# Kernel optimization log

Measured on AMD Instinct MI355X. Metric: run time of the kernel, lower is better.

## Reference

```python
import jax, jax.numpy as jnp
import numpy as np

N = 20000      # total nodes
E = 320000     # edges before self loops
G = 64         # graphs in the batch
H = 8          # attention heads
NEG_SLOPE = 0.2
EPS = 1e-5


def _gatv2(x, src, dst, Wl, bl, Wr, br, att, bias, concat):
    # PyG GATv2Conv: xl = lin_l(x) (source/messages), xr = lin_r(x) (target)
    heads, C = att.shape
    xl = (x @ Wl + bl).reshape(-1, heads, C)
    xr = (x @ Wr + br).reshape(-1, heads, C)
    e = jax.nn.leaky_relu(xl[src] + xr[dst], NEG_SLOPE)          # [E', H, C]
    a = jnp.einsum('ehc,hc->eh', e, att)                          # [E', H]
    amax = jax.ops.segment_max(a, dst, num_segments=N)
    a = jnp.exp(a - amax[dst])
    a = a / jax.ops.segment_sum(a, dst, num_segments=N)[dst]
    out = jax.ops.segment_sum(xl[src] * a[..., None], dst, num_segments=N)
    out = out.reshape(-1, heads * C) if concat else out.mean(axis=1)
    return out + bias


def _graphnorm(x, batch, w, b, ms):
    cnt = jnp.maximum(jax.ops.segment_sum(jnp.ones((x.shape[0],), x.dtype), batch, num_segments=G), 1.0)[:, None]
    mean = jax.ops.segment_sum(x, batch, num_segments=G) / cnt
    out = x - mean[batch] * ms
    var = jax.ops.segment_sum(out * out, batch, num_segments=G) / cnt
    return w * out / jnp.sqrt(var + EPS)[batch] + b


def _mean_pool(x, batch):
    cnt = jnp.maximum(jax.ops.segment_sum(jnp.ones((x.shape[0],), x.dtype), batch, num_segments=G), 1.0)[:, None]
    return jax.ops.segment_sum(x, batch, num_segments=G) / cnt


def setup_inputs():
    key = jax.random.key(0)
    ks = iter(jax.random.split(key, 40))

    def gl(shape, scale=0.05):
        return jax.random.normal(next(ks), shape, jnp.float32) * scale

    inp = {}
    inp['x'] = jax.random.normal(next(ks), (N, 19), jnp.float32)
    inp['edge_index'] = jax.random.randint(next(ks), (2, E), 0, N, jnp.int32)
    inp['batch'] = jnp.sort(jax.random.randint(next(ks), (N,), 0, G, jnp.int32))

    # layer 1: 19 -> (8 heads x 32), concat -> 256
    inp['W1l'] = gl((19, 256)); inp['b1l'] = jnp.zeros((256,), jnp.float32)
    inp['W1r'] = gl((19, 256)); inp['b1r'] = jnp.zeros((256,), jnp.float32)
    inp['att1'] = gl((H, 32)); inp['bias1'] = jnp.zeros((256,), jnp.float32)
    inp['gn1_w'] = jnp.ones((256,), jnp.float32); inp['gn1_b'] = jnp.zeros((256,), jnp.float32); inp['gn1_ms'] = jnp.ones((256,), jnp.float32)

    inp['W2l'] = gl((256, 128)); inp['b2l'] = jnp.zeros((128,), jnp.float32)
    inp['W2r'] = gl((256, 128)); inp['b2r'] = jnp.zeros((128,), jnp.float32)
    inp['att2'] = gl((H, 16)); inp['bias2'] = jnp.zeros((128,), jnp.float32)
    inp['gn2_w'] = jnp.ones((128,), jnp.float32); inp['gn2_b'] = jnp.zeros((128,), jnp.float32); inp['gn2_ms'] = jnp.ones((128,), jnp.float32)

    inp['W3l'] = gl((128, 64)); inp['b3l'] = jnp.zeros((64,), jnp.float32)
    inp['W3r'] = gl((128, 64)); inp['b3r'] = jnp.zeros((64,), jnp.float32)
    inp['att3'] = gl((H, 8)); inp['bias3'] = jnp.zeros((8,), jnp.float32)
    inp['gn3_w'] = jnp.ones((8,), jnp.float32); inp['gn3_b'] = jnp.zeros((8,), jnp.float32); inp['gn3_ms'] = jnp.ones((8,), jnp.float32)

    inp['lin_w'] = gl((8, 4)); inp['lin_b'] = jnp.zeros((4,), jnp.float32)
    return inp


def reference(x, edge_index, batch, W1l, b1l, W1r, b1r, att1, bias1, gn1_w, gn1_b, gn1_ms,
              W2l, b2l, W2r, b2r, att2, bias2, gn2_w, gn2_b, gn2_ms,
              W3l, b3l, W3r, b3r, att3, bias3, gn3_w, gn3_b, gn3_ms, lin_w, lin_b):
    loop = jnp.arange(N, dtype=edge_index.dtype)  # GATv2Conv add_self_loops=True
    src = jnp.concatenate([edge_index[0], loop])
    dst = jnp.concatenate([edge_index[1], loop])

    h = _gatv2(x, src, dst, W1l, b1l, W1r, b1r, att1, bias1, True)
    h = jax.nn.relu(_graphnorm(h, batch, gn1_w, gn1_b, gn1_ms))
    h = _gatv2(h, src, dst, W2l, b2l, W2r, b2r, att2, bias2, True)
    h = jax.nn.relu(_graphnorm(h, batch, gn2_w, gn2_b, gn2_ms))
    h = _gatv2(h, src, dst, W3l, b3l, W3r, b3r, att3, bias3, False)
    h = jax.nn.relu(_graphnorm(h, batch, gn3_w, gn3_b, gn3_ms))

    features = _mean_pool(h, batch)        # [G, 8]
    logits = features @ lin_w + lin_b      # [G, 4]
    return (logits, features)
```

## Files before the change

kernel.cpp:

```cpp
#include <hip/hip_runtime.h>
#include <math.h>

#define NN 20000
#define EE 320000
#define GG 64
#define HH 8
#define EPSV 1e-5f

static inline unsigned int gridFor(long n, int b){ return (unsigned int)((n + b - 1)/b); }

typedef __attribute__((ext_vector_type(8))) short short8;
typedef __attribute__((ext_vector_type(4))) float f32x4;
typedef unsigned short ushort_t;

__global__ void k_deg(const int* __restrict__ edst, int* __restrict__ deg){
    int e = blockIdx.x*blockDim.x + threadIdx.x;
    if (e < EE) atomicAdd(&deg[edst[e]], 1);
}

__global__ void k_scan(const int* __restrict__ deg, int* __restrict__ indptr){
    __shared__ int partial[1024];
    const int CH = (NN + 1023)/1024;
    int t = threadIdx.x;
    int base = t*CH;
    int vals[CH];
    int sum = 0;
    for (int i = 0; i < CH; ++i){
        int v = (base+i < NN) ? deg[base+i] : 0;
        vals[i] = sum; sum += v;
    }
    partial[t] = sum;
    __syncthreads();
    for (int off = 1; off < 1024; off <<= 1){
        int v = (t >= off) ? partial[t-off] : 0;
        __syncthreads();
        partial[t] += v;
        __syncthreads();
    }
    int prefix = (t > 0) ? partial[t-1] : 0;
    for (int i = 0; i < CH; ++i)
        if (base+i < NN) indptr[base+i] = prefix + vals[i];
    if (t == 1023) indptr[NN] = prefix + sum;
}

__global__ void k_scatter(const int* __restrict__ esrc, const int* __restrict__ edst,
                          const int* __restrict__ indptr, int* __restrict__ cursor,
                          int* __restrict__ srclist){
    int e = blockIdx.x*blockDim.x + threadIdx.x;
    if (e >= EE) return;
    int d = edst[e];
    int pos = atomicAdd(&cursor[d], 1);
    srclist[indptr[d] + pos] = esrc[e];
}

__global__ void k_bounds(const int* __restrict__ batch, int* __restrict__ gstart, int* __restrict__ gend){
    int i = blockIdx.x*blockDim.x + threadIdx.x;
    if (i >= NN) return;
    int b = batch[i];
    if (i == 0 || batch[i-1] != b) gstart[b] = i;
    if (i == NN-1 || batch[i+1] != b) gend[b] = i+1;
}

__device__ __forceinline__ float asf(unsigned int u){
    union{unsigned int i; float f;} c; c.i = u; return c.f;
}
__device__ __forceinline__ ushort_t f2bf(float x){
    unsigned u = __float_as_uint(x);
    unsigned r = u + 0x7FFFu + ((u >> 16) & 1u);
    return (ushort_t)(r >> 16);
}
__device__ __forceinline__ void split_bf16(float x, short& hi, short& lo){
    unsigned u = __float_as_uint(x);
    unsigned r = u + 0x7FFFu + ((u >> 16) & 1u);
    hi = (short)(r >> 16);
    float hf = asf(((unsigned)(unsigned short)hi) << 16);
    float res = x - hf;
    unsigned u2 = __float_as_uint(res);
    unsigned r2 = u2 + 0x7FFFu + ((u2 >> 16) & 1u);
    lo = (short)(r2 >> 16);
}

#define SA 40

template<bool NORM>
__global__ __launch_bounds__(256)
void k_gemm_mfma(const float* __restrict__ h,
                 const float* __restrict__ Wl, const float* __restrict__ bl,
                 const float* __restrict__ Wr, const float* __restrict__ br,
                 const float* __restrict__ gmu, const float* __restrict__ ginv,
                 const float* __restrict__ nw, const float* __restrict__ nb,
                 const int* __restrict__ batch,
                 ushort_t* __restrict__ xlb, float* __restrict__ xr,
                 int K, int HC){
    __shared__ short Ahi[64*SA], Alo[64*SA], Bhi[64*SA], Blo[64*SA];
    const int tid  = threadIdx.x;
    const int lane = tid & 63;
    const int wave = tid >> 6;
    const int m0   = blockIdx.x * 64;
    const int n0g  = blockIdx.y * 64;
    const bool right = (n0g >= HC);
    const float* W  = right ? Wr : Wl;
    const float* bv = right ? br : bl;
    const int nbase = right ? (n0g - HC) : n0g;

    const int wr = (wave & 1) * 32;
    const int wc = (wave >> 1) * 32;

    f32x4 acc[2][2] = {};

    const int sm = tid & 63;
    const int sq = tid >> 6;
    const bool kvec = ((K & 7) == 0);

    for (int k0 = 0; k0 < K; k0 += 32){
        {
            int gm = m0 + sm;
            int kb = k0 + sq*8;
            float v[8];
            if (gm < NN && kvec && kb + 8 <= K){
                const float* src = h + (long)gm*K + kb;
                float4 t0 = *(const float4*)src;
                float4 t1 = *(const float4*)(src+4);
                v[0]=t0.x; v[1]=t0.y; v[2]=t0.z; v[3]=t0.w;
                v[4]=t1.x; v[5]=t1.y; v[6]=t1.z; v[7]=t1.w;
            } else {
                const float* src = h + (long)gm*K + kb;
                #pragma unroll
                for (int j = 0; j < 8; ++j)
                    v[j] = (gm < NN && kb + j < K) ? src[j] : 0.f;
            }
            if (NORM && gm < NN){
                int g = batch[gm];
                const float* mu = gmu + (long)g*K;
                const float* iv = ginv + (long)g*K;
                #pragma unroll
                for (int j = 0; j < 8; ++j){
                    int c = kb + j;
                    float t = (v[j] - mu[c]) * iv[c] * nw[c] + nb[c];
                    v[j] = fmaxf(t, 0.f);
                }
            }
            short hi[8], lo[8];
            #pragma unroll
            for (int j = 0; j < 8; ++j) split_bf16(v[j], hi[j], lo[j]);
            *(short8*)&Ahi[sm*SA + sq*8] = *(short8*)hi;
            *(short8*)&Alo[sm*SA + sq*8] = *(short8*)lo;
        }
        {
            int n = sm;
            float v[8];
            #pragma unroll
            for (int j = 0; j < 8; ++j){
                int gk = k0 + sq*8 + j;
                v[j] = (gk < K) ? W[(long)gk*HC + nbase + n] : 0.f;
            }
            short hi[8], lo[8];
            #pragma unroll
            for (int j = 0; j < 8; ++j) split_bf16(v[j], hi[j], lo[j]);
            *(short8*)&Bhi[n*SA + sq*8] = *(short8*)hi;
            *(short8*)&Blo[n*SA + sq*8] = *(short8*)lo;
        }
        __syncthreads();

        const int fm = lane & 15;
        const int fk = (lane >> 4) * 8;
        short8 ah0 = *(short8*)&Ahi[(wr+fm)*SA + fk];
        short8 ah1 = *(short8*)&Ahi[(wr+16+fm)*SA + fk];
        short8 al0 = *(short8*)&Alo[(wr+fm)*SA + fk];
        short8 al1 = *(short8*)&Alo[(wr+16+fm)*SA + fk];
        short8 bh0 = *(short8*)&Bhi[(wc+fm)*SA + fk];
        short8 bh1 = *(short8*)&Bhi[(wc+16+fm)*SA + fk];
        short8 bl0 = *(short8*)&Blo[(wc+fm)*SA + fk];
        short8 bl1 = *(short8*)&Blo[(wc+16+fm)*SA + fk];

        acc[0][0] = __builtin_amdgcn_mfma_f32_16x16x32_bf16(al0, bh0, acc[0][0], 0,0,0);
        acc[0][0] = __builtin_amdgcn_mfma_f32_16x16x32_bf16(ah0, bl0, acc[0][0], 0,0,0);
        acc[0][0] = __builtin_amdgcn_mfma_f32_16x16x32_bf16(ah0, bh0, acc[0][0], 0,0,0);
        acc[0][1] = __builtin_amdgcn_mfma_f32_16x16x32_bf16(al0, bh1, acc[0][1], 0,0,0);
        acc[0][1] = __builtin_amdgcn_mfma_f32_16x16x32_bf16(ah0, bl1, acc[0][1], 0,0,0);
        acc[0][1] = __builtin_amdgcn_mfma_f32_16x16x32_bf16(ah0, bh1, acc[0][1], 0,0,0);
        acc[1][0] = __builtin_amdgcn_mfma_f32_16x16x32_bf16(al1, bh0, acc[1][0], 0,0,0);
        acc[1][0] = __builtin_amdgcn_mfma_f32_16x16x32_bf16(ah1, bl0, acc[1][0], 0,0,0);
        acc[1][0] = __builtin_amdgcn_mfma_f32_16x16x32_bf16(ah1, bh0, acc[1][0], 0,0,0);
        acc[1][1] = __builtin_amdgcn_mfma_f32_16x16x32_bf16(al1, bh1, acc[1][1], 0,0,0);
        acc[1][1] = __builtin_amdgcn_mfma_f32_16x16x32_bf16(ah1, bl1, acc[1][1], 0,0,0);
        acc[1][1] = __builtin_amdgcn_mfma_f32_16x16x32_bf16(ah1, bh1, acc[1][1], 0,0,0);

        __syncthreads();
    }

    #pragma unroll
    for (int i = 0; i < 2; ++i){
        int row0 = m0 + wr + i*16 + (lane >> 4)*4;
        #pragma unroll
        for (int j = 0; j < 2; ++j){
            int col = wc + j*16 + (lane & 15);
            float bb = bv[nbase + col];
            #pragma unroll
            for (int r = 0; r < 4; ++r){
                int gm = row0 + r;
                if (gm >= NN) continue;
                float v = acc[i][j][r] + bb;
                if (right) xr[(long)gm*HC + nbase + col] = v;
                else       xlb[(long)gm*HC + nbase + col] = f2bf(v);
            }
        }
    }
}

template<int VEC> struct VT;
template<> struct VT<1>{ using T = float;  };
template<> struct VT<2>{ using T = float2; };
template<> struct VT<4>{ using T = float4; };

template<int VEC> struct BF;
template<> struct BF<1>{
    static __device__ __forceinline__ float load(const ushort_t* p){
        return asf(((unsigned)*p) << 16);
    }
};
template<> struct BF<2>{
    static __device__ __forceinline__ float2 load(const ushort_t* p){
        unsigned u = *(const unsigned*)p;
        return make_float2(asf(u << 16), asf(u & 0xFFFF0000u));
    }
};
template<> struct BF<4>{
    static __device__ __forceinline__ float4 load(const ushort_t* p){
        uint2 u = *(const uint2*)p;
        return make_float4(asf(u.x << 16), asf(u.x & 0xFFFF0000u),
                           asf(u.y << 16), asf(u.y & 0xFFFF0000u));
    }
};

__device__ __forceinline__ float lrelu(float z){ return z > 0.f ? z : 0.2f*z; }

__device__ __forceinline__ float edot(float xv, float xr, float at){
    return lrelu(xv + xr) * at;
}
__device__ __forceinline__ float edot(float2 xv, float2 xr, float2 at){
    return lrelu(xv.x+xr.x)*at.x + lrelu(xv.y+xr.y)*at.y;
}
__device__ __forceinline__ float edot(float4 xv, float4 xr, float4 at){
    return lrelu(xv.x+xr.x)*at.x + lrelu(xv.y+xr.y)*at.y
         + lrelu(xv.z+xr.z)*at.z + lrelu(xv.w+xr.w)*at.w;
}
__device__ __forceinline__ void efma(float& o, float p, float xv){ o = fmaf(p,xv,o); }
__device__ __forceinline__ void efma(float2& o, float p, float2 xv){
    o.x = fmaf(p,xv.x,o.x); o.y = fmaf(p,xv.y,o.y);
}
__device__ __forceinline__ void efma(float4& o, float p, float4 xv){
    o.x = fmaf(p,xv.x,o.x); o.y = fmaf(p,xv.y,o.y);
    o.z = fmaf(p,xv.z,o.z); o.w = fmaf(p,xv.w,o.w);
}
__device__ __forceinline__ float escale(float o, float s, float b){ return fmaf(o,s,b); }
__device__ __forceinline__ float2 escale(float2 o, float s, float2 b){
    return make_float2(fmaf(o.x,s,b.x), fmaf(o.y,s,b.y));
}
__device__ __forceinline__ float4 escale(float4 o, float s, float4 b){
    return make_float4(fmaf(o.x,s,b.x), fmaf(o.y,s,b.y), fmaf(o.z,s,b.z), fmaf(o.w,s,b.w));
}

__device__ __forceinline__ float red8(float v){
    v += __shfl_xor(v, 1);
    v += __shfl_xor(v, 2);
    v += __shfl_xor(v, 4);
    return v;
}

template<int VEC, bool MEAN>
__global__ __launch_bounds__(256)
void k_gat_w(const int* __restrict__ indptr, const int* __restrict__ srclist,
             const ushort_t* __restrict__ xlb, const float* __restrict__ xr,
             const float* __restrict__ att, const float* __restrict__ bias,
             float* __restrict__ val){
    using V = typename VT<VEC>::T;
    constexpr int HC = 64*VEC;
    const int lane = threadIdx.x & 63;
    const int d = blockIdx.x*4 + (threadIdx.x >> 6);
    const int co = lane*VEC;

    V xrd = *(const V*)&xr[(long)d*HC + co];
    V at  = *(const V*)&att[co];
    V xls = BF<VEC>::load(xlb + (long)d*HC + co);

    float m0 = red8(edot(xls, xrd, at));
    float l = 1.0f;
    V o = xls;

    int j = indptr[d], end = indptr[d+1];
    for (; j + 8 <= end; j += 8){
        int s0 = srclist[j+0], s1 = srclist[j+1], s2 = srclist[j+2], s3 = srclist[j+3];
        int s4 = srclist[j+4], s5 = srclist[j+5], s6 = srclist[j+6], s7 = srclist[j+7];
        V x0 = BF<VEC>::load(xlb + (long)s0*HC + co);
        V x1 = BF<VEC>::load(xlb + (long)s1*HC + co);
        V x2 = BF<VEC>::load(xlb + (long)s2*HC + co);
        V x3 = BF<VEC>::load(xlb + (long)s3*HC + co);
        V x4 = BF<VEC>::load(xlb + (long)s4*HC + co);
        V x5 = BF<VEC>::load(xlb + (long)s5*HC + co);
        V x6 = BF<VEC>::load(xlb + (long)s6*HC + co);
        V x7 = BF<VEC>::load(xlb + (long)s7*HC + co);
        float a0 = red8(edot(x0, xrd, at));
        float a1 = red8(edot(x1, xrd, at));
        float a2 = red8(edot(x2, xrd, at));
        float a3 = red8(edot(x3, xrd, at));
        float a4 = red8(edot(x4, xrd, at));
        float a5 = red8(edot(x5, xrd, at));
        float a6 = red8(edot(x6, xrd, at));
        float a7 = red8(edot(x7, xrd, at));
        float p0 = __expf(a0 - m0), p1 = __expf(a1 - m0);
        float p2 = __expf(a2 - m0), p3 = __expf(a3 - m0);
        float p4 = __expf(a4 - m0), p5 = __expf(a5 - m0);
        float p6 = __expf(a6 - m0), p7 = __expf(a7 - m0);
        l += ((p0+p1)+(p2+p3)) + ((p4+p5)+(p6+p7));
        efma(o, p0, x0); efma(o, p1, x1); efma(o, p2, x2); efma(o, p3, x3);
        efma(o, p4, x4); efma(o, p5, x5); efma(o, p6, x6); efma(o, p7, x7);
    }
    for (; j < end; j += 4){
        int m = end - j;
        int s0 = srclist[j];
        int s1 = (m > 1) ? srclist[j+1] : s0;
        int s2 = (m > 2) ? srclist[j+2] : s0;
        int s3 = (m > 3) ? srclist[j+3] : s0;
        V x0 = BF<VEC>::load(xlb + (long)s0*HC + co);
        V x1 = BF<VEC>::load(xlb + (long)s1*HC + co);
        V x2 = BF<VEC>::load(xlb + (long)s2*HC + co);
        V x3 = BF<VEC>::load(xlb + (long)s3*HC + co);
        float a0 = red8(edot(x0, xrd, at));
        float a1 = red8(edot(x1, xrd, at));
        float a2 = red8(edot(x2, xrd, at));
        float a3 = red8(edot(x3, xrd, at));
        float p0 = __expf(a0 - m0);
        float p1 = __expf(a1 - m0);
        float p2 = __expf(a2 - m0);
        float p3 = __expf(a3 - m0);
        l += p0; efma(o, p0, x0);
        if (m > 1){ l += p1; efma(o, p1, x1); }
        if (m > 2){ l += p2; efma(o, p2, x2); }
        if (m > 3){ l += p3; efma(o, p3, x3); }
    }
    float invl = 1.0f / l;
    if (!MEAN){
        V bv = *(const V*)&bias[co];
        *(V*)&val[(long)d*HC + co] = escale(o, invl, bv);
    } else {
        float r = ((float&)o) * invl;
        r += __shfl_xor(r, 8);
        r += __shfl_xor(r, 16);
        r += __shfl_xor(r, 32);
        if (lane < 8) val[(long)d*8 + lane] = r*0.125f + bias[lane];
    }
}

template<int F>
__global__ void k_gn_partial(const float* __restrict__ val,
                             const int* __restrict__ gstart, const int* __restrict__ gend,
                             float* __restrict__ gsum, float* __restrict__ gsq){
    int g = blockIdx.x, ch = blockIdx.y, nch = gridDim.y;
    int c = threadIdx.x;
    int s = gstart[g], e = gend[g];
    float sum = 0.f, sq = 0.f;
    for (int i = s + ch; i < e; i += nch){
        float v = val[(long)i*F + c];
        sum += v; sq += v*v;
    }
    if (sum != 0.f || sq != 0.f){
        atomicAdd(&gsum[g*F + c], sum);
        atomicAdd(&gsq[g*F + c], sq);
    }
}

__global__ void k_gn_finalize(const float* __restrict__ gsum, const float* __restrict__ gsq,
                              const int* __restrict__ gstart, const int* __restrict__ gend,
                              const float* __restrict__ ms,
                              float* __restrict__ gmu, float* __restrict__ ginv, int F){
    int idx = blockIdx.x*blockDim.x + threadIdx.x;
    if (idx >= GG*F) return;
    int g = idx / F, c = idx - g*F;
    int cnti = gend[g] - gstart[g];
    float cn = cnti > 0 ? (float)cnti : 1.f;
    float mean = gsum[idx] / cn;
    float mu = mean * ms[c];
    float var = gsq[idx]/cn - 2.f*mu*mean + mu*mu;
    gmu[idx]  = mu;
    ginv[idx] = rsqrtf(var + EPSV);
}

__global__ void k_gn_stats8(const float* __restrict__ val,
                            const int* __restrict__ gstart, const int* __restrict__ gend,
                            const float* __restrict__ ms,
                            float* __restrict__ gmu, float* __restrict__ ginv){
    const int F = 8;
    int g = blockIdx.x;
    int t = threadIdx.x;
    int c = t % F, r = t / F;
    int s = gstart[g], e = gend[g];
    float sum = 0.f, sq = 0.f;
    for (int i = s + r; i < e; i += 8){
        float v = val[(long)i*F + c];
        sum += v; sq += v*v;
    }
    #pragma unroll
    for (int mask = 8; mask < 64; mask <<= 1){
        sum += __shfl_xor(sum, mask, 64);
        sq  += __shfl_xor(sq,  mask, 64);
    }
    if (r == 0){
        int cnti = e - s;
        float cn = cnti > 0 ? (float)cnti : 1.f;
        float mean = sum / cn;
        float mu = mean * ms[c];
        float var = sq/cn - 2.f*mu*mean + mu*mu;
        gmu[g*F + c]  = mu;
        ginv[g*F + c] = rsqrtf(var + EPSV);
    }
}

__global__ void k_pool_gn(const float* __restrict__ D,
                          const int* __restrict__ gstart, const int* __restrict__ gend,
                          const float* __restrict__ gmu, const float* __restrict__ ginv,
                          const float* __restrict__ w, const float* __restrict__ b,
                          float* __restrict__ outFeat){
    int g = blockIdx.x;
    int t = threadIdx.x;
    int c = t & 7, r = t >> 3;
    int s = gstart[g], e = gend[g];
    float mu = gmu[g*8 + c], iv = ginv[g*8 + c], wc = w[c], bc = b[c];
    float sum = 0.f;
    for (int i = s + r; i < e; i += 8){
        float v = (D[(long)i*8 + c] - mu) * iv * wc + bc;
        sum += fmaxf(v, 0.f);
    }
    sum += __shfl_xor(sum, 8, 64);
    sum += __shfl_xor(sum, 16, 64);
    sum += __shfl_xor(sum, 32, 64);
    if (t < 8){
        int cnti = e - s;
        float cn = cnti > 0 ? (float)cnti : 1.f;
        outFeat[g*8 + t] = sum / cn;
    }
}

__global__ void k_logits(const float* __restrict__ feat, const float* __restrict__ lw,
                         const float* __restrict__ lb, float* __restrict__ outLog){
    int idx = blockIdx.x*blockDim.x + threadIdx.x;
    if (idx >= GG*4) return;
    int g = idx >> 2, j = idx & 3;
    float a = lb[j];
    for (int c = 0; c < 8; ++c) a += feat[g*8 + c] * lw[c*4 + j];
    outLog[idx] = a;
}

extern "C" void kernel_launch(void* const* d_in, const int* in_sizes, int n_in,
                              void* d_out, int out_size, void* d_ws, size_t ws_size,
                              hipStream_t stream) {
    const float* x     = (const float*)d_in[0];
    const int*   ei    = (const int*)  d_in[1];
    const int*   batch = (const int*)  d_in[2];
    const float* W1l = (const float*)d_in[3];  const float* b1l = (const float*)d_in[4];
    const float* W1r = (const float*)d_in[5];  const float* b1r = (const float*)d_in[6];
    const float* att1= (const float*)d_in[7];  const float* bias1=(const float*)d_in[8];
    const float* g1w = (const float*)d_in[9];  const float* g1b = (const float*)d_in[10];
    const float* g1m = (const float*)d_in[11];
    const float* W2l = (const float*)d_in[12]; const float* b2l = (const float*)d_in[13];
    const float* W2r = (const float*)d_in[14]; const float* b2r = (const float*)d_in[15];
    const float* att2= (const float*)d_in[16]; const float* bias2=(const float*)d_in[17];
    const float* g2w = (const float*)d_in[18]; const float* g2b = (const float*)d_in[19];
    const float* g2m = (const float*)d_in[20];
    const float* W3l = (const float*)d_in[21]; const float* b3l = (const float*)d_in[22];
    const float* W3r = (const float*)d_in[23]; const float* b3r = (const float*)d_in[24];
    const float* att3= (const float*)d_in[25]; const float* bias3=(const float*)d_in[26];
    const float* g3w = (const float*)d_in[27]; const float* g3b = (const float*)d_in[28];
    const float* g3m = (const float*)d_in[29];
    const float* lin_w=(const float*)d_in[30]; const float* lin_b=(const float*)d_in[31];

    const int* esrc = ei;
    const int* edst = ei + EE;

    float* ws = (float*)d_ws;
    int*   cursor  = (int*)(ws + 0);
    int*   indptr  = (int*)(ws + 20480);
    int*   srclist = (int*)(ws + 40960);
    int*   gstart  = (int*)(ws + 361472);
    int*   gend    = (int*)(ws + 361984);
    float* gmu     = ws + 362496;
    float* ginv    = ws + 378880;
    float* gsumP   = ws + 395264;
    float* gsqP    = ws + 411648;
    ushort_t* Bb = (ushort_t*)(ws + 428032);
    float* Cb = ws + 2988032;
    float* D  = ws + 8108032;

    const int TB = 256;
    const int MBm = (NN + 63)/64;
    const int NCH = 32;

    hipMemsetAsync(cursor, 0, NN*sizeof(int), stream);
    k_deg<<<gridFor(EE, TB), TB, 0, stream>>>(edst, cursor);
    k_scan<<<1, 1024, 0, stream>>>(cursor, indptr);
    hipMemsetAsync(cursor, 0, NN*sizeof(int), stream);
    k_scatter<<<gridFor(EE, TB), TB, 0, stream>>>(esrc, edst, indptr, cursor, srclist);
    k_bounds<<<gridFor(NN, TB), TB, 0, stream>>>(batch, gstart, gend);

    k_gemm_mfma<false><<<dim3(MBm, 8), 256, 0, stream>>>(x, W1l, b1l, W1r, b1r,
        nullptr, nullptr, nullptr, nullptr, nullptr, Bb, Cb, 19, 256);
    k_gat_w<4, false><<<NN/4, 256, 0, stream>>>(indptr, srclist, Bb, Cb, att1, bias1, D);
    hipMemsetAsync(gsumP, 0, 2*GG*256*sizeof(float), stream);
    k_gn_partial<256><<<dim3(GG, NCH), 256, 0, stream>>>(D, gstart, gend, gsumP, gsqP);
    k_gn_finalize<<<gridFor(GG*256, TB), TB, 0, stream>>>(gsumP, gsqP, gstart, gend, g1m, gmu, ginv, 256);

    k_gemm_mfma<true><<<dim3(MBm, 4), 256, 0, stream>>>(D, W2l, b2l, W2r, b2r,
        gmu, ginv, g1w, g1b, batch, Bb, Cb, 256, 128);
    k_gat_w<2, false><<<NN/4, 256, 0, stream>>>(indptr, srclist, Bb, Cb, att2, bias2, D);
    hipMemsetAsync(gsumP, 0, 2*GG*256*sizeof(float), stream);
    k_gn_partial<128><<<dim3(GG, NCH), 128, 0, stream>>>(D, gstart, gend, gsumP, gsqP);
    k_gn_finalize<<<gridFor(GG*128, TB), TB, 0, stream>>>(gsumP, gsqP, gstart, gend, g2m, gmu, ginv, 128);

    k_gemm_mfma<true><<<dim3(MBm, 2), 256, 0, stream>>>(D, W3l, b3l, W3r, b3r,
        gmu, ginv, g2w, g2b, batch, Bb, Cb, 128, 64);
    k_gat_w<1, true><<<NN/4, 256, 0, stream>>>(indptr, srclist, Bb, Cb, att3, bias3, D);
    k_gn_stats8<<<GG, 64, 0, stream>>>(D, gstart, gend, g3m, gmu, ginv);

    float* outLog  = (float*)d_out;
    float* outFeat = outLog + GG*4;
    k_pool_gn<<<GG, 64, 0, stream>>>(D, gstart, gend, gmu, ginv, g3w, g3b, outFeat);
    k_logits<<<1, 256, 0, stream>>>(outFeat, lin_w, lin_b, outLog);
}
```

Measured before the change: 363.8 us.

## Pre-split weights into MFMA fragment layout and widen GEMM N-tile to 128

Adds a weight-prep kernel that splits the weights into bf16 hi/lo parts once and stores them already in MFMA fragment order, so the GEMM reads B fragments straight from global memory instead of re-splitting them and staging them through shared memory in every block. The GEMM tile grows to 64x128 with each wave computing 32x64, halving the grid and the repeated A-tile conversion and normalization work. The costs are three extra small launches, more accumulator registers, and B loads that are uncached by LDS and repeated across row blocks.

New measurement: 345.4 us. 5.1% less time.

```diff
diff --git a/kernel.cpp b/kernel.cpp
--- a/kernel.cpp
+++ b/kernel.cpp
@@ -80,54 +80,68 @@
     lo = (short)(r2 >> 16);
 }
 
-#define SA 40
+__global__ void k_wprep(const float* __restrict__ Wl, const float* __restrict__ Wr,
+                        ushort_t* __restrict__ Whi, ushort_t* __restrict__ Wlo,
+                        int K, int Kp, int HC){
+    int octs = Kp >> 3;
+    int t = blockIdx.x*blockDim.x + threadIdx.x;
+    if (t >= 2*HC*octs) return;
+    int n = t / octs, ko = t - n*octs;
+    int kb = ko*8;
+    const float* W = (n < HC) ? (Wl + n) : (Wr + (n - HC));
+    short hi[8], lo[8];
+    #pragma unroll
+    for (int j = 0; j < 8; ++j){
+        int k = kb + j;
+        float v = (k < K) ? W[(long)k*HC] : 0.f;
+        split_bf16(v, hi[j], lo[j]);
+    }
+    long base = (((long)(n>>4)*(Kp>>5) + (kb>>5))*64 + (n&15) + 16*((kb>>3)&3))*8;
+    *(short8*)&Whi[base] = *(short8*)hi;
+    *(short8*)&Wlo[base] = *(short8*)lo;
+}
 
 template<bool NORM>
 __global__ __launch_bounds__(256)
 void k_gemm_mfma(const float* __restrict__ h,
-                 const float* __restrict__ Wl, const float* __restrict__ bl,
-                 const float* __restrict__ Wr, const float* __restrict__ br,
+                 const ushort_t* __restrict__ Whi, const ushort_t* __restrict__ Wlo,
+                 const float* __restrict__ bl, const float* __restrict__ br,
                  const float* __restrict__ gmu, const float* __restrict__ ginv,
                  const float* __restrict__ nw, const float* __restrict__ nb,
                  const int* __restrict__ batch,
                  ushort_t* __restrict__ xlb, float* __restrict__ xr,
-                 int K, int HC){
-    __shared__ short Ahi[64*SA], Alo[64*SA], Bhi[64*SA], Blo[64*SA];
+                 int K, int Kp, int HC){
+    __shared__ short Ahi[64*32], Alo[64*32];
     const int tid  = threadIdx.x;
     const int lane = tid & 63;
     const int wave = tid >> 6;
     const int m0   = blockIdx.x * 64;
-    const int n0g  = blockIdx.y * 64;
-    const bool right = (n0g >= HC);
-    const float* W  = right ? Wr : Wl;
-    const float* bv = right ? br : bl;
-    const int nbase = right ? (n0g - HC) : n0g;
-
-    const int wr = (wave & 1) * 32;
-    const int wc = (wave >> 1) * 32;
-
-    f32x4 acc[2][2] = {};
-
-    const int sm = tid & 63;
-    const int sq = tid >> 6;
-    const bool kvec = ((K & 7) == 0);
-
-    for (int k0 = 0; k0 < K; k0 += 32){
+    const int n0   = blockIdx.y * 128;
+    const int wr   = (wave & 1) * 32;
+    const int wcg  = (wave >> 1) * 64;
+    const int kblocks = Kp >> 5;
+
+    const int srow = tid >> 2;
+    const int soct = tid & 3;
+
+    f32x4 acc[2][4] = {};
+
+    for (int kb = 0; kb < kblocks; ++kb){
+        int k0 = kb*32;
         {
-            int gm = m0 + sm;
-            int kb = k0 + sq*8;
+            int gm = m0 + srow;
+            int kbase = k0 + soct*8;
             float v[8];
-            if (gm < NN && kvec && kb + 8 <= K){
-                const float* src = h + (long)gm*K + kb;
+            const float* src = h + (long)gm*K + kbase;
+            if (gm < NN && kbase + 8 <= K){
                 float4 t0 = *(const float4*)src;
                 float4 t1 = *(const float4*)(src+4);
                 v[0]=t0.x; v[1]=t0.y; v[2]=t0.z; v[3]=t0.w;
                 v[4]=t1.x; v[5]=t1.y; v[6]=t1.z; v[7]=t1.w;
             } else {
-                const float* src = h + (long)gm*K + kb;
                 #pragma unroll
                 for (int j = 0; j < 8; ++j)
-                    v[j] = (gm < NN && kb + j < K) ? src[j] : 0.f;
+                    v[j] = (gm < NN && kbase + j < K) ? src[j] : 0.f;
             }
             if (NORM && gm < NN){
                 int g = batch[gm];
@@ -135,7 +149,7 @@
                 const float* iv = ginv + (long)g*K;
                 #pragma unroll
                 for (int j = 0; j < 8; ++j){
-                    int c = kb + j;
+                    int c = kbase + j;
                     float t = (v[j] - mu[c]) * iv[c] * nw[c] + nb[c];
                     v[j] = fmaxf(t, 0.f);
                 }
@@ -143,49 +157,36 @@
             short hi[8], lo[8];
             #pragma unroll
             for (int j = 0; j < 8; ++j) split_bf16(v[j], hi[j], lo[j]);
-            *(short8*)&Ahi[sm*SA + sq*8] = *(short8*)hi;
-            *(short8*)&Alo[sm*SA + sq*8] = *(short8*)lo;
-        }
-        {
-            int n = sm;
-            float v[8];
-            #pragma unroll
-            for (int j = 0; j < 8; ++j){
-                int gk = k0 + sq*8 + j;
-                v[j] = (gk < K) ? W[(long)gk*HC + nbase + n] : 0.f;
-            }
-            short hi[8], lo[8];
-            #pragma unroll
-            for (int j = 0; j < 8; ++j) split_bf16(v[j], hi[j], lo[j]);
-            *(short8*)&Bhi[n*SA + sq*8] = *(short8*)hi;
-            *(short8*)&Blo[n*SA + sq*8] = *(short8*)lo;
+            long off = ((long)(srow>>4)*64 + (srow&15) + 16*soct)*8;
+            *(short8*)&Ahi[off] = *(short8*)hi;
+            *(short8*)&Alo[off] = *(short8*)lo;
         }
         __syncthreads();
 
-        const int fm = lane & 15;
-        const int fk = (lane >> 4) * 8;
-        short8 ah0 = *(short8*)&Ahi[(wr+fm)*SA + fk];
-        short8 ah1 = *(short8*)&Ahi[(wr+16+fm)*SA + fk];
-        short8 al0 = *(short8*)&Alo[(wr+fm)*SA + fk];
-        short8 al1 = *(short8*)&Alo[(wr+16+fm)*SA + fk];
-        short8 bh0 = *(short8*)&Bhi[(wc+fm)*SA + fk];
-        short8 bh1 = *(short8*)&Bhi[(wc+16+fm)*SA + fk];
-        short8 bl0 = *(short8*)&Blo[(wc+fm)*SA + fk];
-        short8 bl1 = *(short8*)&Blo[(wc+16+fm)*SA + fk];
-
-        acc[0][0] = __builtin_amdgcn_mfma_f32_16x16x32_bf16(al0, bh0, acc[0][0], 0,0,0);
-        acc[0][0] = __builtin_amdgcn_mfma_f32_16x16x32_bf16(ah0, bl0, acc[0][0], 0,0,0);
-        acc[0][0] = __builtin_amdgcn_mfma_f32_16x16x32_bf16(ah0, bh0, acc[0][0], 0,0,0);
-        acc[0][1] = __builtin_amdgcn_mfma_f32_16x16x32_bf16(al0, bh1, acc[0][1], 0,0,0);
-        acc[0][1] = __builtin_amdgcn_mfma_f32_16x16x32_bf16(ah0, bl1, acc[0][1], 0,0,0);
-        acc[0][1] = __builtin_amdgcn_mfma_f32_16x16x32_bf16(ah0, bh1, acc[0][1], 0,0,0);
-        acc[1][0] = __builtin_amdgcn_mfma_f32_16x16x32_bf16(al1, bh0, acc[1][0], 0,0,0);
-        acc[1][0] = __builtin_amdgcn_mfma_f32_16x16x32_bf16(ah1, bl0, acc[1][0], 0,0,0);
-        acc[1][0] = __builtin_amdgcn_mfma_f32_16x16x32_bf16(ah1, bh0, acc[1][0], 0,0,0);
-        acc[1][1] = __builtin_amdgcn_mfma_f32_16x16x32_bf16(al1, bh1, acc[1][1], 0,0,0);
-        acc[1][1] = __builtin_amdgcn_mfma_f32_16x16x32_bf16(ah1, bl1, acc[1][1], 0,0,0);
-        acc[1][1] = __builtin_amdgcn_mfma_f32_16x16x32_bf16(ah1, bh1, acc[1][1], 0,0,0);
-
+        int rb0 = wr >> 4;
+        short8 ah0 = *(short8*)&Ahi[((rb0  )*64 + lane)*8];
+        short8 ah1 = *(short8*)&Ahi[((rb0+1)*64 + lane)*8];
+        short8 al0 = *(short8*)&Alo[((rb0  )*64 + lane)*8];
+        short8 al1 = *(short8*)&Alo[((rb0+1)*64 + lane)*8];
+
+        short8 bh[4], bl_[4];
+        #pragma unroll
+        for (int j = 0; j < 4; ++j){
+            int n = n0 + wcg + j*16;
+            long bbase = (((long)(n>>4)*kblocks + kb)*64 + lane)*8;
+            bh[j]  = *(const short8*)&Whi[bbase];
+            bl_[j] = *(const short8*)&Wlo[bbase];
+        }
+
+        #pragma unroll
+        for (int j = 0; j < 4; ++j){
+            acc[0][j] = __builtin_amdgcn_mfma_f32_16x16x32_bf16(al0, bh[j],  acc[0][j], 0,0,0);
+            acc[0][j] = __builtin_amdgcn_mfma_f32_16x16x32_bf16(ah0, bl_[j], acc[0][j], 0,0,0);
+            acc[0][j] = __builtin_amdgcn_mfma_f32_16x16x32_bf16(ah0, bh[j],  acc[0][j], 0,0,0);
+            acc[1][j] = __builtin_amdgcn_mfma_f32_16x16x32_bf16(al1, bh[j],  acc[1][j], 0,0,0);
+            acc[1][j] = __builtin_amdgcn_mfma_f32_16x16x32_bf16(ah1, bl_[j], acc[1][j], 0,0,0);
+            acc[1][j] = __builtin_amdgcn_mfma_f32_16x16x32_bf16(ah1, bh[j],  acc[1][j], 0,0,0);
+        }
         __syncthreads();
     }
 
@@ -193,16 +194,16 @@
     for (int i = 0; i < 2; ++i){
         int row0 = m0 + wr + i*16 + (lane >> 4)*4;
         #pragma unroll
-        for (int j = 0; j < 2; ++j){
-            int col = wc + j*16 + (lane & 15);
-            float bb = bv[nbase + col];
+        for (int j = 0; j < 4; ++j){
+            int n = n0 + wcg + j*16 + (lane & 15);
+            float bb = (n < HC) ? bl[n] : br[n - HC];
             #pragma unroll
             for (int r = 0; r < 4; ++r){
                 int gm = row0 + r;
                 if (gm >= NN) continue;
                 float v = acc[i][j][r] + bb;
-                if (right) xr[(long)gm*HC + nbase + col] = v;
-                else       xlb[(long)gm*HC + nbase + col] = f2bf(v);
+                if (n < HC) xlb[(long)gm*HC + n] = f2bf(v);
+                else        xr[(long)gm*HC + (n - HC)] = v;
             }
         }
     }
@@ -487,13 +488,23 @@
     float* ginv    = ws + 378880;
     float* gsumP   = ws + 395264;
     float* gsqP    = ws + 411648;
-    ushort_t* Bb = (ushort_t*)(ws + 428032);
-    float* Cb = ws + 2988032;
-    float* D  = ws + 8108032;
+    ushort_t* W1hi = (ushort_t*)(ws + 428032);
+    ushort_t* W1lo = (ushort_t*)(ws + 436224);
+    ushort_t* W2hi = (ushort_t*)(ws + 444416);
+    ushort_t* W2lo = (ushort_t*)(ws + 477184);
+    ushort_t* W3hi = (ushort_t*)(ws + 509952);
+    ushort_t* W3lo = (ushort_t*)(ws + 518144);
+    ushort_t* Bb = (ushort_t*)(ws + 526336);
+    float* Cb = ws + 3086336;
+    float* D  = ws + 8206336;
 
     const int TB = 256;
     const int MBm = (NN + 63)/64;
     const int NCH = 32;
+
+    k_wprep<<<gridFor(512*4,  TB), TB, 0, stream>>>(W1l, W1r, W1hi, W1lo, 19, 32, 256);
+    k_wprep<<<gridFor(256*32, TB), TB, 0, stream>>>(W2l, W2r, W2hi, W2lo, 256, 256, 128);
+    k_wprep<<<gridFor(128*16, TB), TB, 0, stream>>>(W3l, W3r, W3hi, W3lo, 128, 128, 64);
 
     hipMemsetAsync(cursor, 0, NN*sizeof(int), stream);
     k_deg<<<gridFor(EE, TB), TB, 0, stream>>>(edst, cursor);
@@ -502,22 +513,22 @@
     k_scatter<<<gridFor(EE, TB), TB, 0, stream>>>(esrc, edst, indptr, cursor, srclist);
     k_bounds<<<gridFor(NN, TB), TB, 0, stream>>>(batch, gstart, gend);
 
-    k_gemm_mfma<false><<<dim3(MBm, 8), 256, 0, stream>>>(x, W1l, b1l, W1r, b1r,
-        nullptr, nullptr, nullptr, nullptr, nullptr, Bb, Cb, 19, 256);
+    k_gemm_mfma<false><<<dim3(MBm, 4), 256, 0, stream>>>(x, W1hi, W1lo, b1l, b1r,
+        nullptr, nullptr, nullptr, nullptr, nullptr, Bb, Cb, 19, 32, 256);
     k_gat_w<4, false><<<NN/4, 256, 0, stream>>>(indptr, srclist, Bb, Cb, att1, bias1, D);
     hipMemsetAsync(gsumP, 0, 2*GG*256*sizeof(float), stream);
     k_gn_partial<256><<<dim3(GG, NCH), 256, 0, stream>>>(D, gstart, gend, gsumP, gsqP);
     k_gn_finalize<<<gridFor(GG*256, TB), TB, 0, stream>>>(gsumP, gsqP, gstart, gend, g1m, gmu, ginv, 256);
 
-    k_gemm_mfma<true><<<dim3(MBm, 4), 256, 0, stream>>>(D, W2l, b2l, W2r, b2r,
-        gmu, ginv, g1w, g1b, batch, Bb, Cb, 256, 128);
+    k_gemm_mfma<true><<<dim3(MBm, 2), 256, 0, stream>>>(D, W2hi, W2lo, b2l, b2r,
+        gmu, ginv, g1w, g1b, batch, Bb, Cb, 256, 256, 128);
     k_gat_w<2, false><<<NN/4, 256, 0, stream>>>(indptr, srclist, Bb, Cb, att2, bias2, D);
     hipMemsetAsync(gsumP, 0, 2*GG*256*sizeof(float), stream);
     k_gn_partial<128><<<dim3(GG, NCH), 128, 0, stream>>>(D, gstart, gend, gsumP, gsqP);
     k_gn_finalize<<<gridFor(GG*128, TB), TB, 0, stream>>>(gsumP, gsqP, gstart, gend, g2m, gmu, ginv, 128);
 
-    k_gemm_mfma<true><<<dim3(MBm, 2), 256, 0, stream>>>(D, W3l, b3l, W3r, b3r,
-        gmu, ginv, g2w, g2b, batch, Bb, Cb, 128, 64);
+    k_gemm_mfma<true><<<dim3(MBm, 1), 256, 0, stream>>>(D, W3hi, W3lo, b3l, b3r,
+        gmu, ginv, g2w, g2b, batch, Bb, Cb, 128, 128, 64);
     k_gat_w<1, true><<<NN/4, 256, 0, stream>>>(indptr, srclist, Bb, Cb, att3, bias3, D);
     k_gn_stats8<<<GG, 64, 0, stream>>>(D, gstart, gend, g3m, gmu, ginv);
 
```
